# Kernel optimization log

Measured on AMD Instinct MI355X. Metric: run time of the kernel, lower is better.

The kernel has to match this reference:

```python
import jax, jax.numpy as jnp
import numpy as np
from jax import lax

B, T, V, D = 32, 719, 6000, 256  # batch, sentence_length, num_word, embedding_dim
EPS = 1e-5  # BatchNorm eps


def setup_inputs() -> dict:
    key = jax.random.key(0)
    ks = jax.random.split(key, 10)
    s = 0.05
    board = jax.random.normal(ks[0], (B, 19, 19), jnp.float32)
    comment = jax.random.randint(ks[1], (B, T), 0, V)
    comment = comment.at[:, 400:].set(-1)  # -1 padding as in the original data
    return dict(
        board=board,
        comment=comment,
        conv_k=jax.random.normal(ks[2], (1, 1, 3, 3), jnp.float32) * s,
        conv_b=jnp.zeros((1,), jnp.float32),
        bn_gamma=jnp.ones((1,), jnp.float32),
        bn_beta=jnp.zeros((1,), jnp.float32),
        embed_table=jax.random.normal(ks[3], (V, D), jnp.float32) * s,
        lin_W=jax.random.normal(ks[4], (D, 361), jnp.float32) * s,
        lin_b=jnp.zeros((D,), jnp.float32),
        Wih=jax.random.normal(ks[5], (4 * D, D), jnp.float32) * s,
        Whh=jax.random.normal(ks[6], (4 * D, D), jnp.float32) * s,
        bih=jnp.zeros((4 * D,), jnp.float32),
        bhh=jnp.zeros((4 * D,), jnp.float32),
        dec_W=jax.random.normal(ks[7], (V, D), jnp.float32) * s,
        dec_b=jnp.zeros((V,), jnp.float32),
    )


def reference(board, comment, conv_k, conv_b, bn_gamma, bn_beta, embed_table,
              lin_W, lin_b, Wih, Whh, bih, bhh, dec_W, dec_b):
    # --- shared conv+BN block (original aliases ONE module 8 times) ---
    def conv_bn(x):  # x: [B,1,19,19]
        y = lax.conv_general_dilated(x, conv_k, (1, 1), 'SAME')
        y = y + conv_b[None, :, None, None]
        # BN in training mode was applied to batches of size 1 -> per-sample
        # normalization over the 19x19 spatial dims.
        m = y.mean(axis=(2, 3), keepdims=True)
        v = ((y - m) ** 2).mean(axis=(2, 3), keepdims=True)
        return (y - m) / jnp.sqrt(v + EPS) * bn_gamma[None, :, None, None] \
               + bn_beta[None, :, None, None]

    x = board[:, None]  # [B,1,19,19]
    d1 = jax.nn.relu(conv_bn(x))
    d2 = d1
    for _ in range(3):  # residual blocks (layers 1..6, all shared weights)
        d1 = jax.nn.relu(conv_bn(d1))
        d1 = conv_bn(d1)
        d1 = jax.nn.relu(d1 + d2)
        d2 = d1
    d1 = jax.nn.relu(conv_bn(d1))  # layer 7
    feat = d1.reshape(B, 361) @ lin_W.T + lin_b  # [B,D]

    def cell(x, h, c):  # PyTorch LSTMCell gate order: i, f, g, o
        g = x @ Wih.T + bih + h @ Whh.T + bhh
        i, f, gg, o = jnp.split(g, 4, axis=-1)
        c = jax.nn.sigmoid(f) * c + jax.nn.sigmoid(i) * jnp.tanh(gg)
        h = jax.nn.sigmoid(o) * jnp.tanh(c)
        return h, c

    zero = jnp.zeros((B, D), feat.dtype)
    h, c = cell(feat, zero, zero)
    out0 = h @ dec_W.T + dec_b  # [B,V]

    def step(carry, idx):  # idx: [B] token ids at this timestep
        h, c = carry
        mask = (idx == -1)[:, None]
        x = jnp.where(mask, jnp.zeros((), feat.dtype),
                      embed_table[jnp.clip(idx, 0, V - 1)])
        h, c = cell(x, h, c)
        return (h, c), h @ dec_W.T + dec_b

    _, outs = lax.scan(step, (h, c), comment[:, 1:].T)  # [T-1,B,V]
    return jnp.concatenate([out0[:, None], jnp.transpose(outs, (1, 0, 2))], axis=1)  # [B,T,V]
```

## Files before the change

### kernel.cpp

```cpp
#include <hip/hip_runtime.h>
#include <hip/hip_bf16.h>
#include <stdint.h>

typedef unsigned short u16;
typedef unsigned int u32;
typedef unsigned long long u64;
typedef float f32x4 __attribute__((ext_vector_type(4)));
typedef float f32x2 __attribute__((ext_vector_type(2)));
typedef u32 u32x4 __attribute__((ext_vector_type(4)));
typedef __bf16 bf16x8 __attribute__((ext_vector_type(8)));

#define MFMA16(A, B, C) __builtin_amdgcn_mfma_f32_16x16x32_bf16((A), (B), (C), 0, 0, 0)

__device__ __forceinline__ u16 f2bf(float f) {
  u32 u = __float_as_uint(f);
  u32 r = (u + 0x7fffu + ((u >> 16) & 1u)) >> 16;
  return (u16)r;
}
__device__ __forceinline__ bf16x8 ld8(const u16* p) {
  return __builtin_bit_cast(bf16x8, *(const u32x4*)p);
}
__device__ __forceinline__ float sigm(float x) { return 1.f / (1.f + __expf(-x)); }
__device__ __forceinline__ float tanh_f(float x) {
  float a = fabsf(x);
  float e = __expf(-2.f * a);
  float r = (1.f - e) / (1.f + e);
  return copysignf(r, x);
}

__global__ __launch_bounds__(256) void castbf(const float* __restrict__ s,
                                              u16* __restrict__ d, int n4) {
  int i = blockIdx.x * 256 + threadIdx.x;
  if (i >= n4) return;
  f32x4 v = *(const f32x4*)(s + (size_t)i * 4);
  union { u16 t[4]; u64 v; } u;
#pragma unroll
  for (int e = 0; e < 4; e++) u.t[e] = f2bf(v[e]);
  *(u64*)(d + (size_t)i * 4) = u.v;
}

__device__ __forceinline__ float cbn_step(float* cur, float* red, int tid, int r, int c,
                                          bool act, const float* kk, float cb, float gm,
                                          float bt, int w, int l) {
  float y = 0.f;
  if (act) {
#pragma unroll
    for (int dr = -1; dr <= 1; dr++) {
#pragma unroll
      for (int dc = -1; dc <= 1; dc++) {
        int rr = r + dr, cc = c + dc;
        if (rr >= 0 && rr < 19 && cc >= 0 && cc < 19)
          y += cur[rr * 19 + cc] * kk[(dr + 1) * 3 + (dc + 1)];
      }
    }
    y += cb;
  }
  float s = act ? y : 0.f;
  float s2 = act ? y * y : 0.f;
#pragma unroll
  for (int o = 32; o >= 1; o >>= 1) {
    s += __shfl_xor(s, o);
    s2 += __shfl_xor(s2, o);
  }
  if (l == 0) { red[w] = s; red[8 + w] = s2; }
  __syncthreads();
  if (tid == 0) {
    float sa = 0.f, sb = 0.f;
    for (int i = 0; i < 6; i++) { sa += red[i]; sb += red[8 + i]; }
    float m = sa * (1.f / 361.f);
    float v = sb * (1.f / 361.f) - m * m;
    red[14] = m;
    red[15] = rsqrtf(v + 1e-5f) * gm;
  }
  __syncthreads();
  float m = red[14], sc = red[15];
  return act ? ((y - m) * sc + bt) : 0.f;
}

__global__ __launch_bounds__(384) void k1_tower(
    const float* __restrict__ board, const float* __restrict__ convk,
    const float* __restrict__ convb, const float* __restrict__ gma,
    const float* __restrict__ bta, const float* __restrict__ linW,
    const float* __restrict__ linb, const float* __restrict__ Wih,
    float* __restrict__ Z0) {
  const int b = blockIdx.x, tid = threadIdx.x;
  const int w = tid >> 6, l = tid & 63;
  __shared__ __align__(16) float cur[361];
  __shared__ __align__(16) float red[16];
  __shared__ __align__(16) float fs[256];
  const bool act = tid < 361;
  const int r = tid / 19, c = tid - r * 19;
  float kk[9];
#pragma unroll
  for (int i = 0; i < 9; i++) kk[i] = convk[i];
  const float cb = convb[0], gm = gma[0], bt = bta[0];
  if (act) cur[tid] = board[b * 361 + tid];
  __syncthreads();

  float v = cbn_step(cur, red, tid, r, c, act, kk, cb, gm, bt, w, l);
  float d2v = fmaxf(v, 0.f);
  if (act) cur[tid] = d2v;
  __syncthreads();
  for (int it = 0; it < 3; it++) {
    v = cbn_step(cur, red, tid, r, c, act, kk, cb, gm, bt, w, l);
    if (act) cur[tid] = fmaxf(v, 0.f);
    __syncthreads();
    v = cbn_step(cur, red, tid, r, c, act, kk, cb, gm, bt, w, l);
    float nv = fmaxf(v + d2v, 0.f);
    if (act) cur[tid] = nv;
    d2v = nv;
    __syncthreads();
  }
  v = cbn_step(cur, red, tid, r, c, act, kk, cb, gm, bt, w, l);
  if (act) cur[tid] = fmaxf(v, 0.f);
  __syncthreads();

  if (tid < 256) {
    float f = linb[tid];
    const float* wr = linW + tid * 361;
    for (int p = 0; p < 361; p++) f += cur[p] * wr[p];
    fs[tid] = f;
  }
  __syncthreads();
  for (int rr = tid; rr < 1024; rr += 384) {
    const float* wr = Wih + rr * 256;
    float z = 0.f;
#pragma unroll 4
    for (int k2 = 0; k2 < 256; k2++) z += fs[k2] * wr[k2];
    Z0[b * 1024 + rr] = z;
  }
}

template <int DEC>
__global__ __launch_bounds__(256) void gemm_k256(
    const u16* __restrict__ A, const u16* __restrict__ W,
    const float* __restrict__ bias, float* __restrict__ outp, int M, int N) {
  __shared__ __align__(16) u16 As[128 * 72];
  __shared__ __align__(16) u16 Ws[128 * 72];
  const int tid = threadIdx.x;
  const int w = tid >> 6, l = tid & 63, ln = l & 15, q = l >> 4;
  const int wm = (w >> 1) * 64, wn = (w & 1) * 64;
  const int m0 = blockIdx.y * 128, n0 = blockIdx.x * 128;
  f32x4 zero4 = {0.f, 0.f, 0.f, 0.f};
  f32x4 acc[4][4];
#pragma unroll
  for (int i = 0; i < 4; i++)
#pragma unroll
    for (int j = 0; j < 4; j++) acc[i][j] = zero4;

  for (int kb = 0; kb < 4; kb++) {
    if (kb) __syncthreads();
#pragma unroll
    for (int i = 0; i < 4; i++) {
      int ch = tid + i * 256;
      int row = ch >> 3, cj = ch & 7;
      int ga = m0 + row; if (ga > M - 1) ga = M - 1;
      int gw = n0 + row; if (gw > N - 1) gw = N - 1;
      if (DEC) {
        const u64* ap = (const u64*)A + (size_t)ga * 128 + kb * 32 + cj * 4;
        u64 w0 = ap[0], w1 = ap[1], w2 = ap[2], w3 = ap[3];
        u32 pk[4] = {(u32)w0, (u32)w1, (u32)w2, (u32)w3};
        *(u32x4*)&As[row * 72 + cj * 8] = *(const u32x4*)pk;
      } else {
        *(u32x4*)&As[row * 72 + cj * 8] = *(const u32x4*)(A + (size_t)ga * 256 + kb * 64 + cj * 8);
      }
      *(u32x4*)&Ws[row * 72 + cj * 8] = *(const u32x4*)(W + (size_t)gw * 256 + kb * 64 + cj * 8);
    }
    __syncthreads();
#pragma unroll
    for (int kk = 0; kk < 2; kk++) {
      bf16x8 af[4], wf[4];
#pragma unroll
      for (int mt = 0; mt < 4; mt++) af[mt] = ld8(&As[(wm + mt * 16 + ln) * 72 + kk * 32 + q * 8]);
#pragma unroll
      for (int nt = 0; nt < 4; nt++) wf[nt] = ld8(&Ws[(wn + nt * 16 + ln) * 72 + kk * 32 + q * 8]);
#pragma unroll
      for (int mt = 0; mt < 4; mt++)
#pragma unroll
        for (int nt = 0; nt < 4; nt++) acc[mt][nt] = MFMA16(af[mt], wf[nt], acc[mt][nt]);
    }
  }
#pragma unroll
  for (int mt = 0; mt < 4; mt++) {
#pragma unroll
    for (int nt = 0; nt < 4; nt++) {
      int n = n0 + wn + nt * 16 + ln;
#pragma unroll
      for (int rr = 0; rr < 4; rr++) {
        int m = m0 + wm + mt * 16 + q * 4 + rr;
        float vv = acc[mt][nt][rr];
        if (m < M && n < N) {
          if (DEC) {
            vv += bias[n];
            int tt = m >> 5, bb = m & 31;
            outp[((size_t)bb * 719 + tt) * 6000 + n] = vv;
          } else {
            outp[(size_t)m * 1024 + n] = vv;
          }
        }
      }
    }
  }
}

__global__ __launch_bounds__(512) void rnn719(
    const float* __restrict__ Whh, const int* __restrict__ cmt,
    const float* __restrict__ Z0, const float* __restrict__ XW,
    const float* __restrict__ bih, const float* __restrict__ bhh,
    u64* __restrict__ Htag) {
  const int tid = threadIdx.x, wg = blockIdx.x;
  const int j0 = wg * 32;
  const int w = tid >> 6, l = tid & 63, ln = l & 15, q = l >> 4;
  const int ntile = w & 1, mpair = w >> 1;
  __shared__ __align__(16) u16 hs[32 * 264];
  __shared__ __align__(16) float gbuf[128 * 33];

  bf16x8 afr[2][8];
#pragma unroll
  for (int mt = 0; mt < 2; mt++) {
    int mu = (mpair * 2 + mt) * 16 + ln;
    int gate = mu >> 5, jj = mu & 31;
    const float* rp = Whh + (size_t)(gate * 256 + j0 + jj) * 256;
#pragma unroll
    for (int kk = 0; kk < 8; kk++) {
      union { u16 t[8]; bf16x8 v; } u;
#pragma unroll
      for (int e = 0; e < 8; e++) u.t[e] = f2bf(rp[kk * 32 + q * 8 + e]);
      afr[mt][kk] = u.v;
    }
  }

  const int gb = tid >> 4;
  const int jp = (tid & 15) * 2;
  float bs[4][2];
#pragma unroll
  for (int gt = 0; gt < 4; gt++) {
    bs[gt][0] = bih[gt * 256 + j0 + jp] + bhh[gt * 256 + j0 + jp];
    bs[gt][1] = bih[gt * 256 + j0 + jp + 1] + bhh[gt * 256 + j0 + jp + 1];
  }
  float c2[2] = {0.f, 0.f};

  const int myword = gb * 128 + wg * 16 + (tid & 15);

  for (int t = 0; t < 719; t++) {
    float zv[4][2];
    const float* base = nullptr;
    if (t == 0) {
      base = Z0 + gb * 1024;
    } else {
      int idx = cmt[gb * 719 + t];
      if (idx >= 0) base = XW + (size_t)idx * 1024;
    }
    if (base) {
#pragma unroll
      for (int gt = 0; gt < 4; gt++) {
        f32x2 v2 = *(const f32x2*)(base + gt * 256 + j0 + jp);
        zv[gt][0] = v2[0]; zv[gt][1] = v2[1];
      }
    } else {
#pragma unroll
      for (int gt = 0; gt < 4; gt++) { zv[gt][0] = 0.f; zv[gt][1] = 0.f; }
    }

    if (t > 0) {
      const u64* hp = Htag + (size_t)(t - 1) * 4096;
      const u32 expt = (u32)t;
      u64 vals[8];
      int guard = 0;
      for (;;) {
        bool ok = true;
#pragma unroll
        for (int i = 0; i < 8; i++)
          vals[i] = __hip_atomic_load(hp + tid + i * 512, __ATOMIC_RELAXED,
                                      __HIP_MEMORY_SCOPE_AGENT);
#pragma unroll
        for (int i = 0; i < 8; i++) ok &= ((u32)(vals[i] >> 32) == expt);
        if (ok) break;
        if (++guard > (1 << 20)) break;
      }
#pragma unroll
      for (int i = 0; i < 8; i++) {
        int ch = tid + i * 512;
        int row = ch >> 7, dp = ch & 127;
        *(u32*)&hs[row * 264 + dp * 2] = (u32)vals[i];
      }
      __syncthreads();
      f32x4 a0 = {0.f, 0.f, 0.f, 0.f}, a1 = a0;
#pragma unroll
      for (int kk = 0; kk < 8; kk++) {
        bf16x8 bfr = ld8(&hs[(ntile * 16 + ln) * 264 + kk * 32 + q * 8]);
        a0 = MFMA16(afr[0][kk], bfr, a0);
        a1 = MFMA16(afr[1][kk], bfr, a1);
      }
#pragma unroll
      for (int rr = 0; rr < 4; rr++) {
        gbuf[((mpair * 2 + 0) * 16 + q * 4 + rr) * 33 + ntile * 16 + ln] = a0[rr];
        gbuf[((mpair * 2 + 1) * 16 + q * 4 + rr) * 33 + ntile * 16 + ln] = a1[rr];
      }
      __syncthreads();
    }

    u32 hpk = 0;
#pragma unroll
    for (int pj = 0; pj < 2; pj++) {
      int j = jp + pj;
      float gi = zv[0][pj] + bs[0][pj];
      float gf = zv[1][pj] + bs[1][pj];
      float gg = zv[2][pj] + bs[2][pj];
      float go = zv[3][pj] + bs[3][pj];
      if (t > 0) {
        gi += gbuf[(j) * 33 + gb];
        gf += gbuf[(32 + j) * 33 + gb];
        gg += gbuf[(64 + j) * 33 + gb];
        go += gbuf[(96 + j) * 33 + gb];
      }
      float ii = sigm(gi);
      float ff = sigm(gf);
      float g2 = tanh_f(gg);
      float oo = sigm(go);
      float cc = ff * c2[pj] + ii * g2;
      c2[pj] = cc;
      float hh = oo * tanh_f(cc);
      hpk |= ((u32)f2bf(hh)) << (16 * pj);
    }
    __hip_atomic_store(Htag + (size_t)t * 4096 + myword,
                       ((u64)(u32)(t + 1) << 32) | (u64)hpk,
                       __ATOMIC_RELAXED, __HIP_MEMORY_SCOPE_AGENT);
  }
}

extern "C" void kernel_launch(void* const* d_in, const int* in_sizes, int n_in,
                              void* d_out, int out_size, void* d_ws, size_t ws_size,
                              hipStream_t stream) {
  const float* board = (const float*)d_in[0];
  const int*   cmt   = (const int*)d_in[1];
  const float* convk = (const float*)d_in[2];
  const float* convb = (const float*)d_in[3];
  const float* gma   = (const float*)d_in[4];
  const float* bta   = (const float*)d_in[5];
  const float* embed = (const float*)d_in[6];
  const float* linW  = (const float*)d_in[7];
  const float* linb  = (const float*)d_in[8];
  const float* Wih   = (const float*)d_in[9];
  const float* Whh   = (const float*)d_in[10];
  const float* bihp  = (const float*)d_in[11];
  const float* bhhp  = (const float*)d_in[12];
  const float* decW  = (const float*)d_in[13];
  const float* decb  = (const float*)d_in[14];

  char* ws = (char*)d_ws;
  float* Z0     = (float*)(ws + 0);
  float* XW     = (float*)(ws + 131072);
  u64*  Htag    = (u64*)(ws + 24707072);
  u16*  embedB  = (u16*)(ws + 48267264);
  u16*  WihB    = (u16*)(ws + 51339264);
  u16*  decWB   = (u16*)(ws + 51863552);

  hipMemsetAsync(Htag, 0, 23560192, stream);
  hipLaunchKernelGGL(castbf, dim3(1500), dim3(256), 0, stream, embed, embedB, 384000);
  hipLaunchKernelGGL(castbf, dim3(256),  dim3(256), 0, stream, Wih,   WihB,   65536);
  hipLaunchKernelGGL(castbf, dim3(1500), dim3(256), 0, stream, decW,  decWB,  384000);
  hipLaunchKernelGGL(k1_tower, dim3(32), dim3(384), 0, stream,
                     board, convk, convb, gma, bta, linW, linb, Wih, Z0);
  hipLaunchKernelGGL((gemm_k256<0>), dim3(8, 47), dim3(256), 0, stream,
                     embedB, WihB, (const float*)nullptr, XW, 6000, 1024);
  hipLaunchKernelGGL(rnn719, dim3(8), dim3(512), 0, stream,
                     Whh, cmt, Z0, XW, bihp, bhhp, Htag);
  hipLaunchKernelGGL((gemm_k256<1>), dim3(47, 180), dim3(256), 0, stream,
                     (const u16*)Htag, decWB, decb, (float*)d_out, 23008, 6000);
  (void)in_sizes; (void)n_in; (void)out_size; (void)ws_size;
}
```

Baseline: 2.717 ms.

## Fuse decoder GEMM into recurrent kernel with flag-gated persistent decode workers

Merges the output projection GEMM into the recurrent kernel. Eight blocks run the LSTM recurrence while 248 extra persistent blocks poll per-timestep tags and Hdone flags, then compute 128x128 decode tiles as soon as the needed hidden states exist. The aim is to hide the large decoder GEMM and its output writes behind the serial recurrence instead of running them afterwards. The costs are spin-waiting, possible contention for CU and memory bandwidth with the latency-critical recurrent blocks, atomic loads for operands, and a bounded spin guard that could break out early and read unfinished hidden states.

```diff
diff --git a/kernel.cpp b/kernel.cpp
--- a/kernel.cpp
+++ b/kernel.cpp
@@ -131,10 +131,9 @@
   }
 }
 
-template <int DEC>
 __global__ __launch_bounds__(256) void gemm_k256(
     const u16* __restrict__ A, const u16* __restrict__ W,
-    const float* __restrict__ bias, float* __restrict__ outp, int M, int N) {
+    float* __restrict__ outp, int M, int N) {
   __shared__ __align__(16) u16 As[128 * 72];
   __shared__ __align__(16) u16 Ws[128 * 72];
   const int tid = threadIdx.x;
@@ -156,14 +155,7 @@
       int row = ch >> 3, cj = ch & 7;
       int ga = m0 + row; if (ga > M - 1) ga = M - 1;
       int gw = n0 + row; if (gw > N - 1) gw = N - 1;
-      if (DEC) {
-        const u64* ap = (const u64*)A + (size_t)ga * 128 + kb * 32 + cj * 4;
-        u64 w0 = ap[0], w1 = ap[1], w2 = ap[2], w3 = ap[3];
-        u32 pk[4] = {(u32)w0, (u32)w1, (u32)w2, (u32)w3};
-        *(u32x4*)&As[row * 72 + cj * 8] = *(const u32x4*)pk;
-      } else {
-        *(u32x4*)&As[row * 72 + cj * 8] = *(const u32x4*)(A + (size_t)ga * 256 + kb * 64 + cj * 8);
-      }
+      *(u32x4*)&As[row * 72 + cj * 8] = *(const u32x4*)(A + (size_t)ga * 256 + kb * 64 + cj * 8);
       *(u32x4*)&Ws[row * 72 + cj * 8] = *(const u32x4*)(W + (size_t)gw * 256 + kb * 64 + cj * 8);
     }
     __syncthreads();
@@ -188,32 +180,28 @@
 #pragma unroll
       for (int rr = 0; rr < 4; rr++) {
         int m = m0 + wm + mt * 16 + q * 4 + rr;
-        float vv = acc[mt][nt][rr];
-        if (m < M && n < N) {
-          if (DEC) {
-            vv += bias[n];
-            int tt = m >> 5, bb = m & 31;
-            outp[((size_t)bb * 719 + tt) * 6000 + n] = vv;
-          } else {
-            outp[(size_t)m * 1024 + n] = vv;
-          }
-        }
-      }
-    }
-  }
-}
-
-__global__ __launch_bounds__(512) void rnn719(
+        if (m < M && n < N) outp[(size_t)m * 1024 + n] = acc[mt][nt][rr];
+      }
+    }
+  }
+}
+
+union __align__(16) SharedU {
+  struct { u16 hs[32 * 264]; float gbuf[128 * 33]; } r;
+  struct { u16 As[128 * 72]; u16 Ws[128 * 72]; } d;
+};
+
+__device__ void rnn_body(SharedU& sm,
     const float* __restrict__ Whh, const int* __restrict__ cmt,
     const float* __restrict__ Z0, const float* __restrict__ XW,
     const float* __restrict__ bih, const float* __restrict__ bhh,
-    u64* __restrict__ Htag) {
+    u64* __restrict__ Htag, u64* __restrict__ Hdone) {
   const int tid = threadIdx.x, wg = blockIdx.x;
   const int j0 = wg * 32;
   const int w = tid >> 6, l = tid & 63, ln = l & 15, q = l >> 4;
   const int ntile = w & 1, mpair = w >> 1;
-  __shared__ __align__(16) u16 hs[32 * 264];
-  __shared__ __align__(16) float gbuf[128 * 33];
+  u16* hs = sm.r.hs;
+  float* gbuf = sm.r.gbuf;
 
   bf16x8 afr[2][8];
 #pragma unroll
@@ -326,6 +314,119 @@
     __hip_atomic_store(Htag + (size_t)t * 4096 + myword,
                        ((u64)(u32)(t + 1) << 32) | (u64)hpk,
                        __ATOMIC_RELAXED, __HIP_MEMORY_SCOPE_AGENT);
+  }
+  asm volatile("s_waitcnt vmcnt(0)" ::: "memory");
+  __syncthreads();
+  if (tid == 0)
+    __hip_atomic_store(Hdone + wg, ((u64)720u << 32), __ATOMIC_RELAXED,
+                       __HIP_MEMORY_SCOPE_AGENT);
+}
+
+__device__ void decode_body(SharedU& sm,
+    const u64* __restrict__ Htag, const u64* __restrict__ Hdone,
+    const u16* __restrict__ W, const float* __restrict__ bias,
+    float* __restrict__ outp, int worker) {
+  const int tid = threadIdx.x;
+  const int w = tid >> 6, l = tid & 63, ln = l & 15, q = l >> 4;
+  const int wm = (w >> 2) * 64, wn = (w & 3) * 32;
+  const int M = 23008, N = 6000;
+  u16* As = sm.d.As;
+  u16* Ws = sm.d.Ws;
+
+  for (int tau = worker; tau < 47 * 180; tau += 248) {
+    const int by = tau / 47, bx = tau - by * 47;
+    const int m0 = by * 128, n0 = bx * 128;
+    int tmax = (m0 + 127) >> 5; if (tmax > 718) tmax = 718;
+
+    if (tid == 0) {
+      int guard = 0;
+      if (tmax < 718) {
+        const u64* sp = Htag + (size_t)(tmax + 1) * 4096;
+        while ((u32)(__hip_atomic_load(sp, __ATOMIC_RELAXED,
+                                       __HIP_MEMORY_SCOPE_AGENT) >> 32) !=
+               (u32)(tmax + 2)) {
+          if (++guard > (1 << 22)) break;
+        }
+      } else {
+        for (int i = 0; i < 8; i++) {
+          guard = 0;
+          while ((u32)(__hip_atomic_load(Hdone + i, __ATOMIC_RELAXED,
+                                         __HIP_MEMORY_SCOPE_AGENT) >> 32) != 720u) {
+            if (++guard > (1 << 22)) break;
+          }
+        }
+      }
+    }
+    __syncthreads();
+
+    f32x4 zero4 = {0.f, 0.f, 0.f, 0.f};
+    f32x4 acc[4][2];
+#pragma unroll
+    for (int i = 0; i < 4; i++) { acc[i][0] = zero4; acc[i][1] = zero4; }
+
+    for (int kb = 0; kb < 4; kb++) {
+      if (kb) __syncthreads();
+#pragma unroll
+      for (int i = 0; i < 2; i++) {
+        int ch = tid + i * 512;
+        int row = ch >> 3, cj = ch & 7;
+        int ga = m0 + row; if (ga > M - 1) ga = M - 1;
+        int gw = n0 + row; if (gw > N - 1) gw = N - 1;
+        const u64* ap = Htag + (size_t)ga * 128 + kb * 32 + cj * 4;
+        u64 w0 = __hip_atomic_load(ap + 0, __ATOMIC_RELAXED, __HIP_MEMORY_SCOPE_AGENT);
+        u64 w1 = __hip_atomic_load(ap + 1, __ATOMIC_RELAXED, __HIP_MEMORY_SCOPE_AGENT);
+        u64 w2 = __hip_atomic_load(ap + 2, __ATOMIC_RELAXED, __HIP_MEMORY_SCOPE_AGENT);
+        u64 w3 = __hip_atomic_load(ap + 3, __ATOMIC_RELAXED, __HIP_MEMORY_SCOPE_AGENT);
+        u32 pk[4] = {(u32)w0, (u32)w1, (u32)w2, (u32)w3};
+        *(u32x4*)&As[row * 72 + cj * 8] = *(const u32x4*)pk;
+        *(u32x4*)&Ws[row * 72 + cj * 8] = *(const u32x4*)(W + (size_t)gw * 256 + kb * 64 + cj * 8);
+      }
+      __syncthreads();
+#pragma unroll
+      for (int kk = 0; kk < 2; kk++) {
+        bf16x8 af[4], wf[2];
+#pragma unroll
+        for (int mt = 0; mt < 4; mt++) af[mt] = ld8(&As[(wm + mt * 16 + ln) * 72 + kk * 32 + q * 8]);
+#pragma unroll
+        for (int nt = 0; nt < 2; nt++) wf[nt] = ld8(&Ws[(wn + nt * 16 + ln) * 72 + kk * 32 + q * 8]);
+#pragma unroll
+        for (int mt = 0; mt < 4; mt++)
+#pragma unroll
+          for (int nt = 0; nt < 2; nt++) acc[mt][nt] = MFMA16(af[mt], wf[nt], acc[mt][nt]);
+      }
+    }
+#pragma unroll
+    for (int mt = 0; mt < 4; mt++) {
+#pragma unroll
+      for (int nt = 0; nt < 2; nt++) {
+        int n = n0 + wn + nt * 16 + ln;
+#pragma unroll
+        for (int rr = 0; rr < 4; rr++) {
+          int m = m0 + wm + mt * 16 + q * 4 + rr;
+          if (m < M && n < N) {
+            float vv = acc[mt][nt][rr] + bias[n];
+            int tt = m >> 5, bb = m & 31;
+            outp[((size_t)bb * 719 + tt) * 6000 + n] = vv;
+          }
+        }
+      }
+    }
+    __syncthreads();
+  }
+}
+
+__global__ __launch_bounds__(512) void rnn719(
+    const float* __restrict__ Whh, const int* __restrict__ cmt,
+    const float* __restrict__ Z0, const float* __restrict__ XW,
+    const float* __restrict__ bih, const float* __restrict__ bhh,
+    u64* __restrict__ Htag, u64* __restrict__ Hdone,
+    const u16* __restrict__ decW, const float* __restrict__ decb,
+    float* __restrict__ outp) {
+  __shared__ SharedU sm;
+  if (blockIdx.x < 8) {
+    rnn_body(sm, Whh, cmt, Z0, XW, bih, bhh, Htag, Hdone);
+  } else {
+    decode_body(sm, Htag, Hdone, decW, decb, outp, blockIdx.x - 8);
   }
 }
 
@@ -352,21 +453,21 @@
   float* Z0     = (float*)(ws + 0);
   float* XW     = (float*)(ws + 131072);
   u64*  Htag    = (u64*)(ws + 24707072);
-  u16*  embedB  = (u16*)(ws + 48267264);
-  u16*  WihB    = (u16*)(ws + 51339264);
-  u16*  decWB   = (u16*)(ws + 51863552);
-
-  hipMemsetAsync(Htag, 0, 23560192, stream);
+  u64*  Hdone   = (u64*)(ws + 48267264);
+  u16*  embedB  = (u16*)(ws + 48267328);
+  u16*  WihB    = (u16*)(ws + 51339328);
+  u16*  decWB   = (u16*)(ws + 51863616);
+
+  hipMemsetAsync(Htag, 0, 23560256, stream);
   hipLaunchKernelGGL(castbf, dim3(1500), dim3(256), 0, stream, embed, embedB, 384000);
   hipLaunchKernelGGL(castbf, dim3(256),  dim3(256), 0, stream, Wih,   WihB,   65536);
   hipLaunchKernelGGL(castbf, dim3(1500), dim3(256), 0, stream, decW,  decWB,  384000);
   hipLaunchKernelGGL(k1_tower, dim3(32), dim3(384), 0, stream,
                      board, convk, convb, gma, bta, linW, linb, Wih, Z0);
-  hipLaunchKernelGGL((gemm_k256<0>), dim3(8, 47), dim3(256), 0, stream,
-                     embedB, WihB, (const float*)nullptr, XW, 6000, 1024);
-  hipLaunchKernelGGL(rnn719, dim3(8), dim3(512), 0, stream,
-                     Whh, cmt, Z0, XW, bihp, bhhp, Htag);
-  hipLaunchKernelGGL((gemm_k256<1>), dim3(47, 180), dim3(256), 0, stream,
-                     (const u16*)Htag, decWB, decb, (float*)d_out, 23008, 6000);
+  hipLaunchKernelGGL(gemm_k256, dim3(8, 47), dim3(256), 0, stream,
+                     embedB, WihB, XW, 6000, 1024);
+  hipLaunchKernelGGL(rnn719, dim3(256), dim3(512), 0, stream,
+                     Whh, cmt, Z0, XW, bihp, bhhp, Htag, Hdone,
+                     decWB, decb, (float*)d_out);
   (void)in_sizes; (void)n_in; (void)out_size; (void)ws_size;
 }
```

Result: faster. 2.528 ms (-7.0%).
